# Kernel tuning notes

Hardware: AMD Instinct MI355X
Metric: run time of the kernel (lower is better)

The kernel has to match this reference:

```python
import jax, jax.numpy as jnp
import numpy as np

N = 12000       # nodes (Hi-C bins, max_num_nodes)
F_IN = 16       # number_genomic_annotations
HID = 4 * F_IN  # conv1 out = 64
NCLUST = 100    # n_clust
E = 384000      # edges (avg degree 32)


def setup_inputs() -> dict:
    key = jax.random.key(0)
    ks = jax.random.split(key, 8)
    x = jax.random.normal(ks[0], (N, F_IN), dtype=jnp.float32)
    edge_index = jax.random.randint(ks[1], (2, E), 0, N)
    edge_attr = jax.random.uniform(ks[2], (E,), dtype=jnp.float32)
    s1 = 1.0 / np.sqrt(F_IN)
    W1_rel = jax.random.uniform(ks[3], (HID, F_IN), minval=-s1, maxval=s1, dtype=jnp.float32)
    W1_root = jax.random.uniform(ks[4], (HID, F_IN), minval=-s1, maxval=s1, dtype=jnp.float32)
    b1 = jnp.zeros((HID,), jnp.float32)
    s2 = 1.0 / np.sqrt(HID)
    W2_rel = jax.random.uniform(ks[5], (NCLUST, HID), minval=-s2, maxval=s2, dtype=jnp.float32)
    W2_root = jax.random.uniform(ks[6], (NCLUST, HID), minval=-s2, maxval=s2, dtype=jnp.float32)
    b2 = jnp.zeros((NCLUST,), jnp.float32)
    return dict(x=x, edge_index=edge_index, edge_attr=edge_attr,
                W1_rel=W1_rel, W1_root=W1_root, b1=b1,
                W2_rel=W2_rel, W2_root=W2_root, b2=b2)


def _graph_conv(x, src, dst, ew, W_rel, W_root, b):
    # PyG GraphConv (aggr='add'): out = lin_rel(sum_j e_ji * x_j) + lin_root(x)
    msg = x[src] * ew[:, None]                       # [E, F]
    aggr = jax.ops.segment_sum(msg, dst, num_segments=N)  # [N, F]
    return aggr @ W_rel.T + b + x @ W_root.T


def reference(x, edge_index, edge_attr, W1_rel, W1_root, b1, W2_rel, W2_root, b2):
    src, dst = edge_index[0], edge_index[1]
    h = _graph_conv(x, src, dst, edge_attr, W1_rel, W1_root, b1)
    h = jax.nn.relu(h)  # dropout is identity in eval mode
    s_out = _graph_conv(h, src, dst, edge_attr, W2_rel, W2_root, b2)  # [N, NCLUST]

    # to_dense_adj (duplicate edges summed)
    adj = jnp.zeros((N, N), x.dtype).at[src, dst].add(edge_attr)  # [N, N]

    # dense_mincut_pool with S = x (as in the original forward), k = F_IN
    s_mc = jax.nn.softmax(x, axis=-1)      # [N, F_IN]
    as_ = adj @ s_mc                        # [N, F_IN]
    out_adj = s_mc.T @ as_                  # [F_IN, F_IN]
    mincut_num = jnp.trace(out_adj)
    d_flat = adj.sum(-1)                    # [N] degree
    mincut_den = jnp.einsum('ik,i,ik->', s_mc, d_flat, s_mc)  # trace(S^T D S)
    mc = -(mincut_num / mincut_den)

    ss = s_mc.T @ s_mc                      # [F_IN, F_IN]
    i_k = jnp.eye(F_IN, dtype=ss.dtype)
    o = jnp.linalg.norm(ss / jnp.linalg.norm(ss) - i_k / jnp.linalg.norm(i_k))

    return jax.nn.softmax(s_out, axis=-1), mc, o
```

## Files before the change

### kernel.cpp

```cpp
#include <hip/hip_runtime.h>
#include <math.h>

#define N_NODES 12000
#define F_INN 16
#define HIDD 64
#define NCLUST 100
#define NEDGE 384000
#define NBLK_N 47
#define CAP 96
#define EPT 4
#define NBLK_E 375
#define NBLK_F1 (N_NODES / 4)
#define NBLK_F2 (N_NODES / 8)

#define NBIN 188
#define BINW 64
#define BCAP 2560
#define STCAP 24

#define OFF_BINCNT  0
#define OFF_SCAL    188
#define ZERO_ELEMS  190
#define OFF_COUNT   192
#define OFF_SSPART  12192
#define OFF_NORM2   24224
#define OFF_W2TREL  36224
#define OFF_W2TROOT 42624
#define OFF_SMC     49024
#define OFF_H       241024
#define OFF_SRCW    1009024
#define OFF_BINBUF  3313024

__global__ void binA_kernel(const float* __restrict__ x, const int* __restrict__ ei,
                            const float* __restrict__ ew, float* __restrict__ smc,
                            float* __restrict__ norm2, int* __restrict__ bincnt,
                            int2* __restrict__ binbuf, const float* __restrict__ W2_rel,
                            const float* __restrict__ W2_root, float* __restrict__ w2t_rel,
                            float* __restrict__ w2t_root) {
    __shared__ int shmA[188 + 188 * STCAP * 2];
    int t = threadIdx.x;
    int b = blockIdx.x;
    if (b < NBLK_E) {
        int* scnt = shmA;
        int2* sbuf = (int2*)(shmA + 188);
        for (int i = t; i < 188; i += 256) scnt[i] = 0;
        __syncthreads();
        int tid = b * 256 + t;
        int e0 = tid * EPT;
        int4 sv = *(const int4*)(ei + e0);
        int4 dv = *(const int4*)(ei + NEDGE + e0);
        float4 wv = *(const float4*)(ew + e0);
        int s[EPT] = {sv.x, sv.y, sv.z, sv.w};
        int d[EPT] = {dv.x, dv.y, dv.z, dv.w};
        float w[EPT] = {wv.x, wv.y, wv.z, wv.w};
#pragma unroll
        for (int i = 0; i < EPT; ++i) {
            int bin = d[i] >> 6;
            int dl = d[i] & 63;
            int2 rec = make_int2(s[i] | (dl << 16), __float_as_int(w[i]));
            int pos = atomicAdd(&scnt[bin], 1);
            if (pos < STCAP) {
                sbuf[bin * STCAP + pos] = rec;
            } else {
                int base = atomicAdd(&bincnt[bin], 1);
                binbuf[bin * BCAP + base] = rec;
            }
        }
        __syncthreads();
        if (t < 188) {
            int k = scnt[t];
            if (k > STCAP) k = STCAP;
            if (k > 0) {
                int base = atomicAdd(&bincnt[t], k);
                for (int i = 0; i < k; ++i) binbuf[t * BCAP + base + i] = sbuf[t * STCAP + i];
            }
        }
    } else if (b < NBLK_E + NBLK_N) {
        int i = (b - NBLK_E) * 256 + t;
        if (i >= N_NODES) return;
        const float4* xr = (const float4*)(x + i * 16);
        float4 r0 = xr[0], r1 = xr[1], r2 = xr[2], r3 = xr[3];
        float v[16] = {r0.x, r0.y, r0.z, r0.w, r1.x, r1.y, r1.z, r1.w,
                       r2.x, r2.y, r2.z, r2.w, r3.x, r3.y, r3.z, r3.w};
        float m = v[0];
#pragma unroll
        for (int k = 1; k < 16; ++k) m = fmaxf(m, v[k]);
        float s = 0.f;
#pragma unroll
        for (int k = 0; k < 16; ++k) { v[k] = __expf(v[k] - m); s += v[k]; }
        float inv = 1.f / s;
        float n2 = 0.f;
#pragma unroll
        for (int k = 0; k < 16; ++k) { v[k] *= inv; n2 += v[k] * v[k]; }
        float4* so = (float4*)(smc + i * 16);
        so[0] = make_float4(v[0], v[1], v[2], v[3]);
        so[1] = make_float4(v[4], v[5], v[6], v[7]);
        so[2] = make_float4(v[8], v[9], v[10], v[11]);
        so[3] = make_float4(v[12], v[13], v[14], v[15]);
        norm2[i] = n2;
    } else {
        float* fl = (float*)shmA;
        const float* src = (b == NBLK_E + NBLK_N) ? W2_rel : W2_root;
        float* dst = (b == NBLK_E + NBLK_N) ? w2t_rel : w2t_root;
        for (int i = t; i < 6400; i += 256) fl[i] = src[i];
        __syncthreads();
        for (int j = t; j < 6400; j += 256) {
            int kk = j / 100, cl = j - kk * 100;
            dst[j] = fl[cl * 64 + kk];
        }
    }
}

__global__ void binB_kernel(const int2* __restrict__ binbuf, const int* __restrict__ bincnt,
                            int* __restrict__ count, int2* __restrict__ srcw,
                            const float* __restrict__ smc, float* __restrict__ sspart,
                            const int* __restrict__ ei, const float* __restrict__ ew,
                            const float* __restrict__ norm2, float* __restrict__ scal) {
    __shared__ int shmB[64 + 64 * CAP * 2];
    int t = threadIdx.x;
    int b = blockIdx.x;
    if (b < NBIN) {
        int* cnt = shmB;
        int2* lbuck = (int2*)(shmB + 64);
        for (int i = t; i < 64; i += 256) cnt[i] = 0;
        __syncthreads();
        int nE = bincnt[b];
        const int2* bp = binbuf + b * BCAP;
        for (int i = t; i < nE; i += 256) {
            int2 rec = bp[i];
            int src = rec.x & 0xFFFF;
            int dl = rec.x >> 16;
            int pos = atomicAdd(&cnt[dl], 1);
            if (pos < CAP) lbuck[dl * CAP + pos] = make_int2(src, rec.y);
        }
        __syncthreads();
        int nbase = b * BINW;
        int nvalid = N_NODES - nbase;
        if (nvalid > BINW) nvalid = BINW;
        if (t < nvalid) count[nbase + t] = cnt[t];
        int lim = nvalid * CAP;
        int2* out = srcw + (size_t)nbase * CAP;
        for (int i = t; i < lim; i += 256) out[i] = lbuck[i];
    } else if (b < NBIN + NBLK_N) {
        int bb = b - NBIN;
        float* rows = (float*)shmB;
        int n = bb * 256 + t;
        float* rp = rows + t * 17;
        if (n < N_NODES) {
            const float4* sr = (const float4*)(smc + n * 16);
            float4 a0 = sr[0], a1 = sr[1], a2v = sr[2], a3 = sr[3];
            rp[0] = a0.x;  rp[1] = a0.y;  rp[2] = a0.z;  rp[3] = a0.w;
            rp[4] = a1.x;  rp[5] = a1.y;  rp[6] = a1.z;  rp[7] = a1.w;
            rp[8] = a2v.x; rp[9] = a2v.y; rp[10] = a2v.z; rp[11] = a2v.w;
            rp[12] = a3.x; rp[13] = a3.y; rp[14] = a3.z; rp[15] = a3.w;
        } else {
#pragma unroll
            for (int k = 0; k < 16; ++k) rp[k] = 0.f;
        }
        __syncthreads();
        int a = t & 15, bq = t >> 4;
        float accs = 0.f;
#pragma unroll 4
        for (int r = 0; r < 256; ++r)
            accs = fmaf(rows[r * 17 + a], rows[r * 17 + bq], accs);
        sspart[bb * 256 + t] = accs;
    } else {
        int tid = (b - NBIN - NBLK_N) * 256 + t;
        int e0 = tid * EPT;
        int4 sv = *(const int4*)(ei + e0);
        int4 dv = *(const int4*)(ei + NEDGE + e0);
        float4 wv = *(const float4*)(ew + e0);
        int s[EPT] = {sv.x, sv.y, sv.z, sv.w};
        int d[EPT] = {dv.x, dv.y, dv.z, dv.w};
        float w[EPT] = {wv.x, wv.y, wv.z, wv.w};
        float np = 0.f, dp = 0.f;
#pragma unroll
        for (int i = 0; i < EPT; ++i) {
            const float4* ps = (const float4*)(smc + s[i] * 16);
            const float4* pd = (const float4*)(smc + d[i] * 16);
            float4 s0 = ps[0], s1 = ps[1], s2 = ps[2], s3 = ps[3];
            float4 d0 = pd[0], d1 = pd[1], d2 = pd[2], d3 = pd[3];
            float dot = s0.x * d0.x + s0.y * d0.y + s0.z * d0.z + s0.w * d0.w +
                        s1.x * d1.x + s1.y * d1.y + s1.z * d1.z + s1.w * d1.w +
                        s2.x * d2.x + s2.y * d2.y + s2.z * d2.z + s2.w * d2.w +
                        s3.x * d3.x + s3.y * d3.y + s3.z * d3.z + s3.w * d3.w;
            np = fmaf(w[i], dot, np);
            dp = fmaf(w[i], norm2[s[i]], dp);
        }
        float* redn = (float*)shmB;
        float* redd = (float*)shmB + 256;
        redn[t] = np;
        redd[t] = dp;
        __syncthreads();
        for (int s2 = 128; s2 > 0; s2 >>= 1) {
            if (t < s2) { redn[t] += redn[t + s2]; redd[t] += redd[t + s2]; }
            __syncthreads();
        }
        if (t == 0) {
            atomicAdd(&scal[0], redn[0]);
            atomicAdd(&scal[1], redd[0]);
        }
    }
}

__global__ void fused1_kernel(const float* __restrict__ x, const int2* __restrict__ srcw,
                              const int* __restrict__ count, const float* __restrict__ W1_rel,
                              const float* __restrict__ W1_root, const float* __restrict__ b1,
                              float* __restrict__ h) {
    __shared__ float shm[2304];
    int t = threadIdx.x;
    int b = blockIdx.x;
    float* wrelT  = shm;
    float* wrootT = shm + 1024;
    float* b1s    = shm + 2048;
    float* aggr   = shm + 2112;
    float* xs     = shm + 2176;
    for (int idx = t; idx < 1024; idx += 256) {
        int f = idx >> 4, k = idx & 15;
        wrelT[(k << 6) + f]  = W1_rel[idx];
        wrootT[(k << 6) + f] = W1_root[idx];
    }
    if (t < 64) b1s[t] = b1[t];
    int w = t >> 6, lane = t & 63;
    int j2 = lane >> 2;
    int q  = lane & 3;
    int n = b * 4 + w;
    int len = count[n];
    const int2* bucket = srcw + n * CAP;
    float4 acc4 = make_float4(0.f, 0.f, 0.f, 0.f);
    for (int k = 0; k < len; k += 32) {
        int ia = k + j2, ib = k + 16 + j2;
        int2 pa = bucket[ia];
        int2 pb = bucket[ib];
        if (ia >= len) pa = make_int2(0, 0);
        if (ib >= len) pb = make_int2(0, 0);
        float4 va = *(const float4*)(x + pa.x * 16 + q * 4);
        float4 vb = *(const float4*)(x + pb.x * 16 + q * 4);
        float wa = __int_as_float(pa.y), wb = __int_as_float(pb.y);
        acc4.x = fmaf(va.x, wa, acc4.x); acc4.y = fmaf(va.y, wa, acc4.y);
        acc4.z = fmaf(va.z, wa, acc4.z); acc4.w = fmaf(va.w, wa, acc4.w);
        acc4.x = fmaf(vb.x, wb, acc4.x); acc4.y = fmaf(vb.y, wb, acc4.y);
        acc4.z = fmaf(vb.z, wb, acc4.z); acc4.w = fmaf(vb.w, wb, acc4.w);
    }
    acc4.x += __shfl_xor(acc4.x, 4);  acc4.y += __shfl_xor(acc4.y, 4);
    acc4.z += __shfl_xor(acc4.z, 4);  acc4.w += __shfl_xor(acc4.w, 4);
    acc4.x += __shfl_xor(acc4.x, 8);  acc4.y += __shfl_xor(acc4.y, 8);
    acc4.z += __shfl_xor(acc4.z, 8);  acc4.w += __shfl_xor(acc4.w, 8);
    acc4.x += __shfl_xor(acc4.x, 16); acc4.y += __shfl_xor(acc4.y, 16);
    acc4.z += __shfl_xor(acc4.z, 16); acc4.w += __shfl_xor(acc4.w, 16);
    acc4.x += __shfl_xor(acc4.x, 32); acc4.y += __shfl_xor(acc4.y, 32);
    acc4.z += __shfl_xor(acc4.z, 32); acc4.w += __shfl_xor(acc4.w, 32);
    if (j2 == 0) *(float4*)(aggr + w * 16 + q * 4) = acc4;
    if (lane < 16) xs[w * 16 + lane] = x[n * 16 + lane];
    __syncthreads();
    float o = b1s[lane];
#pragma unroll
    for (int kk = 0; kk < 16; ++kk)
        o = fmaf(aggr[w * 16 + kk], wrelT[(kk << 6) + lane],
                 fmaf(xs[w * 16 + kk], wrootT[(kk << 6) + lane], o));
    h[n * 64 + lane] = fmaxf(o, 0.f);
}

__global__ __launch_bounds__(512) void fused2_finalize_kernel(
    const float* __restrict__ h, const int2* __restrict__ srcw, const int* __restrict__ count,
    const float* __restrict__ w2t_rel, const float* __restrict__ w2t_root,
    const float* __restrict__ b2, float* __restrict__ out, const float* __restrict__ sspart,
    const float* __restrict__ scal) {
    __shared__ float wsrel[6400];
    __shared__ float a2[8][64], hrow[8][64];
    __shared__ float logits[8][104];
    __shared__ float b2s[104];
    int t = threadIdx.x;
    int b = blockIdx.x;
    if (b < NBLK_F2) {
        for (int i = t; i < 6400; i += 512) wsrel[i] = w2t_rel[i];
        if (t < NCLUST) b2s[t] = b2[t];
        int nn = t >> 6;
        int c = t & 63;
        int eslot = c >> 4;
        int q = c & 15;
        int n = b * 8 + nn;
        int len = count[n];
        const int2* bucket = srcw + n * CAP;
        float4 acc4 = make_float4(0.f, 0.f, 0.f, 0.f);
        for (int k = 0; k < len; k += 32) {
            int i0 = k + eslot,      i1 = k + 4 + eslot;
            int i2 = k + 8 + eslot,  i3 = k + 12 + eslot;
            int i4 = k + 16 + eslot, i5 = k + 20 + eslot;
            int i6 = k + 24 + eslot, i7 = k + 28 + eslot;
            int2 pa = bucket[i0]; int2 pb = bucket[i1];
            int2 pc = bucket[i2]; int2 pd = bucket[i3];
            int2 pe = bucket[i4]; int2 pf = bucket[i5];
            int2 pg = bucket[i6]; int2 ph = bucket[i7];
            if (i0 >= len) pa = make_int2(0, 0);
            if (i1 >= len) pb = make_int2(0, 0);
            if (i2 >= len) pc = make_int2(0, 0);
            if (i3 >= len) pd = make_int2(0, 0);
            if (i4 >= len) pe = make_int2(0, 0);
            if (i5 >= len) pf = make_int2(0, 0);
            if (i6 >= len) pg = make_int2(0, 0);
            if (i7 >= len) ph = make_int2(0, 0);
            float4 va = *(const float4*)(h + pa.x * 64 + q * 4);
            float4 vb = *(const float4*)(h + pb.x * 64 + q * 4);
            float4 vc = *(const float4*)(h + pc.x * 64 + q * 4);
            float4 vd = *(const float4*)(h + pd.x * 64 + q * 4);
            float4 ve = *(const float4*)(h + pe.x * 64 + q * 4);
            float4 vf = *(const float4*)(h + pf.x * 64 + q * 4);
            float4 vg = *(const float4*)(h + pg.x * 64 + q * 4);
            float4 vh = *(const float4*)(h + ph.x * 64 + q * 4);
            float wa = __int_as_float(pa.y), wb = __int_as_float(pb.y);
            float wc = __int_as_float(pc.y), wd = __int_as_float(pd.y);
            float we = __int_as_float(pe.y), wf = __int_as_float(pf.y);
            float wg = __int_as_float(pg.y), wh = __int_as_float(ph.y);
            acc4.x = fmaf(va.x, wa, acc4.x); acc4.y = fmaf(va.y, wa, acc4.y);
            acc4.z = fmaf(va.z, wa, acc4.z); acc4.w = fmaf(va.w, wa, acc4.w);
            acc4.x = fmaf(vb.x, wb, acc4.x); acc4.y = fmaf(vb.y, wb, acc4.y);
            acc4.z = fmaf(vb.z, wb, acc4.z); acc4.w = fmaf(vb.w, wb, acc4.w);
            acc4.x = fmaf(vc.x, wc, acc4.x); acc4.y = fmaf(vc.y, wc, acc4.y);
            acc4.z = fmaf(vc.z, wc, acc4.z); acc4.w = fmaf(vc.w, wc, acc4.w);
            acc4.x = fmaf(vd.x, wd, acc4.x); acc4.y = fmaf(vd.y, wd, acc4.y);
            acc4.z = fmaf(vd.z, wd, acc4.z); acc4.w = fmaf(vd.w, wd, acc4.w);
            acc4.x = fmaf(ve.x, we, acc4.x); acc4.y = fmaf(ve.y, we, acc4.y);
            acc4.z = fmaf(ve.z, we, acc4.z); acc4.w = fmaf(ve.w, we, acc4.w);
            acc4.x = fmaf(vf.x, wf, acc4.x); acc4.y = fmaf(vf.y, wf, acc4.y);
            acc4.z = fmaf(vf.z, wf, acc4.z); acc4.w = fmaf(vf.w, wf, acc4.w);
            acc4.x = fmaf(vg.x, wg, acc4.x); acc4.y = fmaf(vg.y, wg, acc4.y);
            acc4.z = fmaf(vg.z, wg, acc4.z); acc4.w = fmaf(vg.w, wg, acc4.w);
            acc4.x = fmaf(vh.x, wh, acc4.x); acc4.y = fmaf(vh.y, wh, acc4.y);
            acc4.z = fmaf(vh.z, wh, acc4.z); acc4.w = fmaf(vh.w, wh, acc4.w);
        }
        acc4.x += __shfl_xor(acc4.x, 16); acc4.y += __shfl_xor(acc4.y, 16);
        acc4.z += __shfl_xor(acc4.z, 16); acc4.w += __shfl_xor(acc4.w, 16);
        acc4.x += __shfl_xor(acc4.x, 32); acc4.y += __shfl_xor(acc4.y, 32);
        acc4.z += __shfl_xor(acc4.z, 32); acc4.w += __shfl_xor(acc4.w, 32);
        if (eslot == 0) *(float4*)(&a2[nn][q * 4]) = acc4;
        hrow[nn][c] = h[n * 64 + c];
        __syncthreads();
        int g = t >> 7, c2 = t & 127;
        if (c2 < NCLUST) {
            int na = 2 * g, nb2 = 2 * g + 1;
            float s0 = b2s[c2], s1 = s0;
#pragma unroll 8
            for (int kk = 0; kk < 64; ++kk) {
                float wr = wsrel[kk * 100 + c2];
                float wo = w2t_root[kk * 100 + c2];
                s0 = fmaf(a2[na][kk], wr, fmaf(hrow[na][kk], wo, s0));
                s1 = fmaf(a2[nb2][kk], wr, fmaf(hrow[nb2][kk], wo, s1));
            }
            logits[na][c2] = s0;
            logits[nb2][c2] = s1;
        }
        __syncthreads();
        float v0 = logits[nn][c];
        float v1 = (c < NCLUST - 64) ? logits[nn][64 + c] : -INFINITY;
        float m = fmaxf(v0, v1);
#pragma unroll
        for (int off = 32; off > 0; off >>= 1) m = fmaxf(m, __shfl_xor(m, off));
        float e0 = __expf(v0 - m);
        float e1 = (c < NCLUST - 64) ? __expf(v1 - m) : 0.f;
        float s = e0 + e1;
#pragma unroll
        for (int off = 32; off > 0; off >>= 1) s += __shfl_xor(s, off);
        float inv = 1.f / s;
        out[n * NCLUST + c] = e0 * inv;
        if (c < NCLUST - 64) out[n * NCLUST + 64 + c] = e1 * inv;
    } else {
        float* red = wsrel;
        float sv = 0.f;
        if (t < 256)
            for (int bb = 0; bb < NBLK_N; ++bb) sv += sspart[bb * 256 + t];
        red[t] = sv * sv;
        __syncthreads();
        for (int s = 256; s > 0; s >>= 1) {
            if (t < s) red[t] += red[t + s];
            __syncthreads();
        }
        float ssnorm = sqrtf(red[0]);
        __syncthreads();
        float diff = (t < 256) ? (sv / ssnorm - ((t % 17 == 0) ? 0.25f : 0.f)) : 0.f;
        red[t] = diff * diff;
        __syncthreads();
        for (int s = 256; s > 0; s >>= 1) {
            if (t < s) red[t] += red[t + s];
            __syncthreads();
        }
        if (t == 0) {
            out[N_NODES * NCLUST + 0] = -(scal[0] / scal[1]);
            out[N_NODES * NCLUST + 1] = sqrtf(red[0]);
        }
    }
}

extern "C" void kernel_launch(void* const* d_in, const int* in_sizes, int n_in,
                              void* d_out, int out_size, void* d_ws, size_t ws_size,
                              hipStream_t stream) {
    const float* x       = (const float*)d_in[0];
    const int*   ei      = (const int*)d_in[1];
    const float* ew      = (const float*)d_in[2];
    const float* W1_rel  = (const float*)d_in[3];
    const float* W1_root = (const float*)d_in[4];
    const float* b1      = (const float*)d_in[5];
    const float* W2_rel  = (const float*)d_in[6];
    const float* W2_root = (const float*)d_in[7];
    const float* b2      = (const float*)d_in[8];
    float* out = (float*)d_out;
    int*   wsi = (int*)d_ws;

    int*   bincnt  = wsi + OFF_BINCNT;
    float* scal    = (float*)(wsi + OFF_SCAL);
    int*   count   = wsi + OFF_COUNT;
    float* sspart  = (float*)(wsi + OFF_SSPART);
    float* norm2   = (float*)(wsi + OFF_NORM2);
    float* w2trel  = (float*)(wsi + OFF_W2TREL);
    float* w2troot = (float*)(wsi + OFF_W2TROOT);
    float* smc     = (float*)(wsi + OFF_SMC);
    float* h       = (float*)(wsi + OFF_H);
    int2*  srcw    = (int2*)(wsi + OFF_SRCW);
    int2*  binbuf  = (int2*)(wsi + OFF_BINBUF);

    hipMemsetAsync(wsi, 0, ZERO_ELEMS * sizeof(int), stream);
    binA_kernel<<<NBLK_E + NBLK_N + 2, 256, 0, stream>>>(x, ei, ew, smc, norm2, bincnt, binbuf,
                                                         W2_rel, W2_root, w2trel, w2troot);
    binB_kernel<<<NBIN + NBLK_N + NBLK_E, 256, 0, stream>>>(binbuf, bincnt, count, srcw,
                                                            smc, sspart, ei, ew, norm2, scal);
    fused1_kernel<<<NBLK_F1, 256, 0, stream>>>(x, srcw, count, W1_rel, W1_root, b1, h);
    fused2_finalize_kernel<<<NBLK_F2 + 1, 512, 0, stream>>>(h, srcw, count, w2trel, w2troot,
                                                            b2, out, sspart, scal);
}
```

Measured before the change: 90.45 us.

## Fuse layer-1 graph conv into bucket-building kernel using shared-memory buckets

Folds the first GraphConv (gather-aggregate plus dense transform and ReLU) into the per-bin bucketing blocks, so each bin block reads its neighbor lists straight from shared memory instead of rereading them from global memory in a separate kernel. This removes one kernel launch and the global round-trip for the first-layer aggregation, and replaces the shared-memory staging of aggregates with wavefront shuffles. In exchange, only 188 blocks now do the layer-1 work (64 nodes each, 4 waves looping), down from 3000 blocks. That lowers parallelism, and the extra static shared memory per block may reduce occupancy.

Measured after the change: 92.32 us. 1.02x slower.

```diff
diff --git a/kernel.cpp b/kernel.cpp
--- a/kernel.cpp
+++ b/kernel.cpp
@@ -10,9 +10,7 @@
 #define CAP 96
 #define EPT 4
 #define NBLK_E 375
-#define NBLK_F1 (N_NODES / 4)
 #define NBLK_F2 (N_NODES / 8)
-
 #define NBIN 188
 #define BINW 64
 #define BCAP 2560
@@ -111,17 +109,27 @@
     }
 }
 
-__global__ void binB_kernel(const int2* __restrict__ binbuf, const int* __restrict__ bincnt,
-                            int* __restrict__ count, int2* __restrict__ srcw,
-                            const float* __restrict__ smc, float* __restrict__ sspart,
-                            const int* __restrict__ ei, const float* __restrict__ ew,
-                            const float* __restrict__ norm2, float* __restrict__ scal) {
-    __shared__ int shmB[64 + 64 * CAP * 2];
+__global__ void binBF1_kernel(const int2* __restrict__ binbuf, const int* __restrict__ bincnt,
+                              int* __restrict__ count, int2* __restrict__ srcw,
+                              const float* __restrict__ x, const float* __restrict__ W1_rel,
+                              const float* __restrict__ W1_root, const float* __restrict__ b1,
+                              float* __restrict__ h, const float* __restrict__ smc,
+                              float* __restrict__ sspart, const int* __restrict__ ei,
+                              const float* __restrict__ ew, const float* __restrict__ norm2,
+                              float* __restrict__ scal) {
+    __shared__ int shmU[64 + 64 * CAP * 2];
+    __shared__ float wrelT[1024], wrootT[1024], b1s[64];
     int t = threadIdx.x;
     int b = blockIdx.x;
     if (b < NBIN) {
-        int* cnt = shmB;
-        int2* lbuck = (int2*)(shmB + 64);
+        int* cnt = shmU;
+        int2* lbuck = (int2*)(shmU + 64);
+        for (int idx = t; idx < 1024; idx += 256) {
+            int f = idx >> 4, k = idx & 15;
+            wrelT[(k << 6) + f]  = W1_rel[idx];
+            wrootT[(k << 6) + f] = W1_root[idx];
+        }
+        if (t < 64) b1s[t] = b1[t];
         for (int i = t; i < 64; i += 256) cnt[i] = 0;
         __syncthreads();
         int nE = bincnt[b];
@@ -139,11 +147,54 @@
         if (nvalid > BINW) nvalid = BINW;
         if (t < nvalid) count[nbase + t] = cnt[t];
         int lim = nvalid * CAP;
-        int2* out = srcw + (size_t)nbase * CAP;
-        for (int i = t; i < lim; i += 256) out[i] = lbuck[i];
+        int2* outp = srcw + (size_t)nbase * CAP;
+        for (int i = t; i < lim; i += 256) outp[i] = lbuck[i];
+        int w = t >> 6, lane = t & 63;
+        int j2 = lane >> 2;
+        int q  = lane & 3;
+        for (int ni = w; ni < nvalid; ni += 4) {
+            int n = nbase + ni;
+            int len = cnt[ni];
+            const int2* bucket = lbuck + ni * CAP;
+            float4 acc4 = make_float4(0.f, 0.f, 0.f, 0.f);
+            for (int k = 0; k < len; k += 32) {
+                int ia = k + j2, ib = k + 16 + j2;
+                int2 pa = bucket[ia];
+                int2 pb = bucket[ib];
+                if (ia >= len) pa = make_int2(0, 0);
+                if (ib >= len) pb = make_int2(0, 0);
+                float4 va = *(const float4*)(x + pa.x * 16 + q * 4);
+                float4 vb = *(const float4*)(x + pb.x * 16 + q * 4);
+                float wa = __int_as_float(pa.y), wb = __int_as_float(pb.y);
+                acc4.x = fmaf(va.x, wa, acc4.x); acc4.y = fmaf(va.y, wa, acc4.y);
+                acc4.z = fmaf(va.z, wa, acc4.z); acc4.w = fmaf(va.w, wa, acc4.w);
+                acc4.x = fmaf(vb.x, wb, acc4.x); acc4.y = fmaf(vb.y, wb, acc4.y);
+                acc4.z = fmaf(vb.z, wb, acc4.z); acc4.w = fmaf(vb.w, wb, acc4.w);
+            }
+            acc4.x += __shfl_xor(acc4.x, 4);  acc4.y += __shfl_xor(acc4.y, 4);
+            acc4.z += __shfl_xor(acc4.z, 4);  acc4.w += __shfl_xor(acc4.w, 4);
+            acc4.x += __shfl_xor(acc4.x, 8);  acc4.y += __shfl_xor(acc4.y, 8);
+            acc4.z += __shfl_xor(acc4.z, 8);  acc4.w += __shfl_xor(acc4.w, 8);
+            acc4.x += __shfl_xor(acc4.x, 16); acc4.y += __shfl_xor(acc4.y, 16);
+            acc4.z += __shfl_xor(acc4.z, 16); acc4.w += __shfl_xor(acc4.w, 16);
+            acc4.x += __shfl_xor(acc4.x, 32); acc4.y += __shfl_xor(acc4.y, 32);
+            acc4.z += __shfl_xor(acc4.z, 32); acc4.w += __shfl_xor(acc4.w, 32);
+            float xv = (lane < 16) ? x[n * 16 + lane] : 0.f;
+            float o = b1s[lane];
+#define F1STEP(KK, COMP) { float ag = __shfl(acc4.COMP, (KK) >> 2);            \
+                           float xb = __shfl(xv, (KK));                        \
+                           o = fmaf(ag, wrelT[((KK) << 6) + lane],             \
+                                    fmaf(xb, wrootT[((KK) << 6) + lane], o)); }
+            F1STEP(0, x)  F1STEP(1, y)  F1STEP(2, z)  F1STEP(3, w)
+            F1STEP(4, x)  F1STEP(5, y)  F1STEP(6, z)  F1STEP(7, w)
+            F1STEP(8, x)  F1STEP(9, y)  F1STEP(10, z) F1STEP(11, w)
+            F1STEP(12, x) F1STEP(13, y) F1STEP(14, z) F1STEP(15, w)
+#undef F1STEP
+            h[n * 64 + lane] = fmaxf(o, 0.f);
+        }
     } else if (b < NBIN + NBLK_N) {
         int bb = b - NBIN;
-        float* rows = (float*)shmB;
+        float* rows = (float*)shmU;
         int n = bb * 256 + t;
         float* rp = rows + t * 17;
         if (n < N_NODES) {
@@ -187,8 +238,8 @@
             np = fmaf(w[i], dot, np);
             dp = fmaf(w[i], norm2[s[i]], dp);
         }
-        float* redn = (float*)shmB;
-        float* redd = (float*)shmB + 256;
+        float* redn = (float*)shmU;
+        float* redd = (float*)shmU + 256;
         redn[t] = np;
         redd[t] = dp;
         __syncthreads();
@@ -201,64 +252,6 @@
             atomicAdd(&scal[1], redd[0]);
         }
     }
-}
-
-__global__ void fused1_kernel(const float* __restrict__ x, const int2* __restrict__ srcw,
-                              const int* __restrict__ count, const float* __restrict__ W1_rel,
-                              const float* __restrict__ W1_root, const float* __restrict__ b1,
-                              float* __restrict__ h) {
-    __shared__ float shm[2304];
-    int t = threadIdx.x;
-    int b = blockIdx.x;
-    float* wrelT  = shm;
-    float* wrootT = shm + 1024;
-    float* b1s    = shm + 2048;
-    float* aggr   = shm + 2112;
-    float* xs     = shm + 2176;
-    for (int idx = t; idx < 1024; idx += 256) {
-        int f = idx >> 4, k = idx & 15;
-        wrelT[(k << 6) + f]  = W1_rel[idx];
-        wrootT[(k << 6) + f] = W1_root[idx];
-    }
-    if (t < 64) b1s[t] = b1[t];
-    int w = t >> 6, lane = t & 63;
-    int j2 = lane >> 2;
-    int q  = lane & 3;
-    int n = b * 4 + w;
-    int len = count[n];
-    const int2* bucket = srcw + n * CAP;
-    float4 acc4 = make_float4(0.f, 0.f, 0.f, 0.f);
-    for (int k = 0; k < len; k += 32) {
-        int ia = k + j2, ib = k + 16 + j2;
-        int2 pa = bucket[ia];
-        int2 pb = bucket[ib];
-        if (ia >= len) pa = make_int2(0, 0);
-        if (ib >= len) pb = make_int2(0, 0);
-        float4 va = *(const float4*)(x + pa.x * 16 + q * 4);
-        float4 vb = *(const float4*)(x + pb.x * 16 + q * 4);
-        float wa = __int_as_float(pa.y), wb = __int_as_float(pb.y);
-        acc4.x = fmaf(va.x, wa, acc4.x); acc4.y = fmaf(va.y, wa, acc4.y);
-        acc4.z = fmaf(va.z, wa, acc4.z); acc4.w = fmaf(va.w, wa, acc4.w);
-        acc4.x = fmaf(vb.x, wb, acc4.x); acc4.y = fmaf(vb.y, wb, acc4.y);
-        acc4.z = fmaf(vb.z, wb, acc4.z); acc4.w = fmaf(vb.w, wb, acc4.w);
-    }
-    acc4.x += __shfl_xor(acc4.x, 4);  acc4.y += __shfl_xor(acc4.y, 4);
-    acc4.z += __shfl_xor(acc4.z, 4);  acc4.w += __shfl_xor(acc4.w, 4);
-    acc4.x += __shfl_xor(acc4.x, 8);  acc4.y += __shfl_xor(acc4.y, 8);
-    acc4.z += __shfl_xor(acc4.z, 8);  acc4.w += __shfl_xor(acc4.w, 8);
-    acc4.x += __shfl_xor(acc4.x, 16); acc4.y += __shfl_xor(acc4.y, 16);
-    acc4.z += __shfl_xor(acc4.z, 16); acc4.w += __shfl_xor(acc4.w, 16);
-    acc4.x += __shfl_xor(acc4.x, 32); acc4.y += __shfl_xor(acc4.y, 32);
-    acc4.z += __shfl_xor(acc4.z, 32); acc4.w += __shfl_xor(acc4.w, 32);
-    if (j2 == 0) *(float4*)(aggr + w * 16 + q * 4) = acc4;
-    if (lane < 16) xs[w * 16 + lane] = x[n * 16 + lane];
-    __syncthreads();
-    float o = b1s[lane];
-#pragma unroll
-    for (int kk = 0; kk < 16; ++kk)
-        o = fmaf(aggr[w * 16 + kk], wrelT[(kk << 6) + lane],
-                 fmaf(xs[w * 16 + kk], wrootT[(kk << 6) + lane], o));
-    h[n * 64 + lane] = fmaxf(o, 0.f);
 }
 
 __global__ __launch_bounds__(512) void fused2_finalize_kernel(
@@ -421,9 +414,9 @@
     hipMemsetAsync(wsi, 0, ZERO_ELEMS * sizeof(int), stream);
     binA_kernel<<<NBLK_E + NBLK_N + 2, 256, 0, stream>>>(x, ei, ew, smc, norm2, bincnt, binbuf,
                                                          W2_rel, W2_root, w2trel, w2troot);
-    binB_kernel<<<NBIN + NBLK_N + NBLK_E, 256, 0, stream>>>(binbuf, bincnt, count, srcw,
-                                                            smc, sspart, ei, ew, norm2, scal);
-    fused1_kernel<<<NBLK_F1, 256, 0, stream>>>(x, srcw, count, W1_rel, W1_root, b1, h);
+    binBF1_kernel<<<NBIN + NBLK_N + NBLK_E, 256, 0, stream>>>(
+        binbuf, bincnt, count, srcw, x, W1_rel, W1_root, b1, h,
+        smc, sspart, ei, ew, norm2, scal);
     fused2_finalize_kernel<<<NBLK_F2 + 1, 512, 0, stream>>>(h, srcw, count, w2trel, w2troot,
                                                             b2, out, sspart, scal);
 }
```
